# Optimization experiments

Measured on AMD Instinct MI355X. Metric: run time of the kernel, lower is better.

## Reference

```python
import jax, jax.numpy as jnp
import numpy as np

DEPTH = 16
PERCENT = 1.2
MAX_P = 5.0
# ps[t] = clip((t+1)*percent, 0, max_percent), as in the torch __init__
PS = np.clip((np.arange(DEPTH) + 1) * PERCENT, 0.0, MAX_P)


def setup_inputs() -> dict:
    key = jax.random.key(0)
    kx, kA = jax.random.split(key, 2)
    B, M, N = 16384, 256, 1024
    A = jax.random.normal(kA, (M, N), dtype=jnp.float32) / np.sqrt(M)
    # L = max eigenvalue of A^T A (as max_eig in the torch code), scaled by 1.001
    gram = np.asarray(A.T @ A)
    L = float(np.linalg.eigvalsh(gram)[-1]) * 1.001
    # init=True initialization: every bias layer weight is A.T / L, threshold = 1/L
    W = jnp.tile((A.T / L)[None, :, :], (DEPTH, 1, 1))  # [depth, N, M]
    threshold = jnp.ones((DEPTH,), dtype=jnp.float32) / L
    x = jax.random.normal(kx, (B, M), dtype=jnp.float32)
    return {"x": x, "A": A, "W": W, "threshold": threshold}


def _shrink(x, t):
    # soft threshold: sign(x) * max(|x| - t, 0)
    return jnp.sign(x) * jnp.maximum(jnp.abs(x) - t, 0.0)


def _shrinkss(x, t, p):
    # support-selection shrink: entries above both the learned threshold and the
    # per-row (100-p) percentile of |x| pass through untouched; the rest are
    # soft-thresholded. Mask and percentile are detached (no_grad in torch).
    n = x.shape[1]
    idx = int(np.ceil((100.0 - p) / 100.0 * n)) - 1  # static per iteration
    abs_x = jnp.abs(x)
    thresh = jax.lax.stop_gradient(jnp.sort(abs_x, axis=1)[:, idx])  # [B]
    mask = jax.lax.stop_gradient(
        ((abs_x >= t) & (abs_x >= thresh[:, None])).astype(x.dtype)
    )
    return mask * x + _shrink((1.0 - mask) * x, t)


def reference(x, A, W, threshold):
    # x: [B, M], A: [M, N], W: [depth, N, M], threshold: [depth]
    B = x.shape[0]
    N = A.shape[1]
    u = jnp.zeros((B, N), dtype=x.dtype)
    for i in range(DEPTH):
        r = x - u @ A.T                      # residual in measurement space [B, M]
        v = u + r @ W[i].T                   # gradient step via learned bias [B, N]
        u = _shrinkss(v, threshold[i], PS[i])
    return u
```

## Files before the change

### kernel.cpp

```cpp
#include <hip/hip_runtime.h>
#include <hip/hip_bf16.h>

#define B_ROWS 16384
#define M_DIM  256
#define N_DIM  1024
#define DEPTH  16

typedef __attribute__((ext_vector_type(8))) short short8;
typedef __attribute__((ext_vector_type(4))) float f32x4;
typedef __attribute__((ext_vector_type(2))) float f32x2;

#define ATP_OFF_B   0
#define WTP_OFF_B   1572864
#define RP_OFF_B    (1572864 + 25165824)
#define WS_FAST_NEED ((size_t)RP_OFF_B + 25165824)
#define WTP_SLICE   (64 * 8 * 3 * 512)
#define RP_PANEL_US 24576

#define AT_OFF 0
#define WT_OFF (262144)
#define WS_OLD_NEED ((size_t)(262144 + 16 * 262144) * 4)

__device__ __forceinline__ unsigned short bf16r(float f) {
    unsigned u = __float_as_uint(f);
    u += 0x7fffu + ((u >> 16) & 1u);
    return (unsigned short)(u >> 16);
}
__device__ __forceinline__ float bf2f(unsigned short h) {
    return __uint_as_float(((unsigned)h) << 16);
}
__device__ __forceinline__ void split3(float x, unsigned short& h, unsigned short& m,
                                       unsigned short& lo) {
    h = bf16r(x); float r1 = x - bf2f(h);
    m = bf16r(r1); float r2 = r1 - bf2f(m);
    lo = bf16r(r2);
}
__device__ __forceinline__ f32x4 MF(short8 a, short8 b, f32x4 c) {
    return __builtin_amdgcn_mfma_f32_16x16x32_bf16(a, b, c, 0, 0, 0);
}
__device__ __forceinline__ float shrink_one(float v, float t, float thrv) {
    float a = fabsf(v);
    return (a >= thrv) ? v : copysignf(fmaxf(a - t, 0.0f), v);
}

__global__ void prep_a_kernel(const float* __restrict__ A, unsigned short* __restrict__ ATp) {
    int g = blockIdx.x * 256 + threadIdx.x;
    if (g >= 16 * 32 * 64) return;
    int l = g & 63, kc = (g >> 6) & 31, tile = g >> 11;
    int row = tile * 16 + (l & 15);
    int k0 = kc * 32 + ((l >> 4) << 3);
    unsigned short h[8], m[8], lo[8];
#pragma unroll
    for (int j = 0; j < 8; ++j) split3(A[(size_t)row * N_DIM + k0 + j], h[j], m[j], lo[j]);
    size_t base = ((size_t)(tile * 32 + kc) * 3) * 512 + l * 8;
#pragma unroll
    for (int j = 0; j < 8; ++j) {
        ATp[base + j] = h[j];
        ATp[base + 512 + j] = m[j];
        ATp[base + 1024 + j] = lo[j];
    }
}

__global__ void prep_w_kernel(const float* __restrict__ W, unsigned short* __restrict__ WTp) {
    int g = blockIdx.x * 256 + threadIdx.x;
    if (g >= 16 * 64 * 8 * 64) return;
    int l = g & 63, kc = (g >> 6) & 7, tile = (g >> 9) & 63, it = g >> 15;
    int n = tile * 16 + (l & 15);
    int m0 = kc * 32 + ((l >> 4) << 3);
    const float* Wi = W + (size_t)it * N_DIM * M_DIM;
    unsigned short h[8], m[8], lo[8];
#pragma unroll
    for (int j = 0; j < 8; ++j) split3(Wi[(size_t)n * M_DIM + m0 + j], h[j], m[j], lo[j]);
    size_t base = (((size_t)(it * 64 + tile) * 8 + kc) * 3) * 512 + l * 8;
#pragma unroll
    for (int j = 0; j < 8; ++j) {
        WTp[base + j] = h[j];
        WTp[base + 512 + j] = m[j];
        WTp[base + 1024 + j] = lo[j];
    }
}

__global__ void prep_x_kernel(const float* __restrict__ x, unsigned short* __restrict__ RP) {
    int g = blockIdx.x * 256 + threadIdx.x;
    if (g >= 524288) return;
    int l = g & 63, kcp = (g >> 6) & 3, wm = (g >> 8) & 1, c = (g >> 9) & 1, panel = g >> 10;
    int row = panel * 32 + wm * 16 + (l & 15);
    int k0 = c * 128 + kcp * 32 + ((l >> 4) << 3);
    unsigned short h[8], m[8], lo[8];
#pragma unroll
    for (int j = 0; j < 8; ++j) split3(x[(size_t)row * M_DIM + k0 + j], h[j], m[j], lo[j]);
    size_t base = (size_t)panel * RP_PANEL_US + ((((c * 2 + wm) * 4 + kcp) * 3)) * 512 + l * 8;
#pragma unroll
    for (int j = 0; j < 8; ++j) {
        RP[base + j] = h[j];
        RP[base + 512 + j] = m[j];
        RP[base + 1024 + j] = lo[j];
    }
}

__global__ __launch_bounds__(1024)
void spp_kernel(float* __restrict__ UV, const float* __restrict__ thr_all,
                int iter, int kth) {
    const int l = threadIdx.x & 63;
    const int w = threadIdx.x >> 6;
    const int row = blockIdx.x * 16 + w;
    const float t = thr_all[iter];
    float* vp = UV + (size_t)row * N_DIM;
    float v[16]; unsigned key[16];
#pragma unroll
    for (int j = 0; j < 16; ++j) {
        v[j] = vp[l + 64 * j];
        key[j] = __float_as_uint(v[j]) & 0x7fffffffu;
    }
    unsigned p = 0;
#pragma unroll 1
    for (int b = 30; b >= 0; --b) {
        const unsigned cand = p | (1u << b);
        int cnt = 0;
#pragma unroll
        for (int j = 0; j < 16; ++j)
            cnt += __popcll(__ballot(key[j] >= cand));
        if (cnt >= kth) p = cand;
    }
    const float thrv = fmaxf(t, __uint_as_float(p));
#pragma unroll
    for (int j = 0; j < 16; ++j)
        vp[l + 64 * j] = shrink_one(v[j], t, thrv);
}

#define LSTR2 136
#define BUFUS 13056

__global__ __launch_bounds__(1024)
void g1_kernel(const float* __restrict__ UV, const float* __restrict__ x,
               const unsigned short* __restrict__ ATp,
               unsigned short* __restrict__ RP) {
    __align__(16) __shared__ unsigned short smem[2 * BUFUS];
    const int tid = threadIdx.x;
    const int l = tid & 63, w = tid >> 6;
    const int wm = w >> 3, wn = w & 7;
    const int panel = blockIdx.x;
    const int row0 = panel * 32;
    const int arow = 16 * wm + (l & 15);
    const int akl  = (l >> 4) << 3;

    f32x4 acc_hi[2], acc_rest[2];
    double acc64[2][4];
#pragma unroll
    for (int t = 0; t < 2; ++t) {
        acc_hi[t] = (f32x4){0, 0, 0, 0};
        acc_rest[t] = (f32x4){0, 0, 0, 0};
#pragma unroll
        for (int e = 0; e < 4; ++e) acc64[t][e] = 0.0;
    }

    f32x2 st[2];
#pragma unroll
    for (int jj = 0; jj < 2; ++jj) {
        const int idx = tid + 1024 * jj;
        const int r = idx >> 6, kq = idx & 63;
        st[jj] = *(const f32x2*)&UV[(size_t)(row0 + r) * N_DIM + kq * 2];
    }
#pragma unroll
    for (int jj = 0; jj < 2; ++jj) {
        const int idx = tid + 1024 * jj;
        const int r = idx >> 6, kq = idx & 63;
        unsigned short h0, m0, lo0, h1, m1, lo1;
        split3(st[jj].x, h0, m0, lo0);
        split3(st[jj].y, h1, m1, lo1);
        const unsigned off = (unsigned)r * LSTR2 + kq * 2;
        *(unsigned*)&smem[off] = (unsigned)h0 | ((unsigned)h1 << 16);
        *(unsigned*)&smem[4352 + off] = (unsigned)m0 | ((unsigned)m1 << 16);
        *(unsigned*)&smem[8704 + off] = (unsigned)lo0 | ((unsigned)lo1 << 16);
    }
#pragma unroll
    for (int jj = 0; jj < 2; ++jj) {
        const int idx = tid + 1024 * jj;
        const int r = idx >> 6, kq = idx & 63;
        st[jj] = *(const f32x2*)&UV[(size_t)(row0 + r) * N_DIM + 128 + kq * 2];
    }
    __syncthreads();

    for (int c = 0; c < 8; ++c) {
        const unsigned bb = (unsigned)(c & 1) * BUFUS;
        const unsigned nb = (unsigned)((c + 1) & 1) * BUFUS;
        if (c < 7) {
#pragma unroll
            for (int jj = 0; jj < 2; ++jj) {
                const int idx = tid + 1024 * jj;
                const int r = idx >> 6, kq = idx & 63;
                unsigned short h0, m0, lo0, h1, m1, lo1;
                split3(st[jj].x, h0, m0, lo0);
                split3(st[jj].y, h1, m1, lo1);
                const unsigned off = (unsigned)r * LSTR2 + kq * 2;
                *(unsigned*)&smem[nb + off] = (unsigned)h0 | ((unsigned)h1 << 16);
                *(unsigned*)&smem[nb + 4352 + off] = (unsigned)m0 | ((unsigned)m1 << 16);
                *(unsigned*)&smem[nb + 8704 + off] = (unsigned)lo0 | ((unsigned)lo1 << 16);
            }
        }
        if (c < 6) {
#pragma unroll
            for (int jj = 0; jj < 2; ++jj) {
                const int idx = tid + 1024 * jj;
                const int r = idx >> 6, kq = idx & 63;
                st[jj] = *(const f32x2*)&UV[(size_t)(row0 + r) * N_DIM + (c + 2) * 128 + kq * 2];
            }
        }
#pragma unroll
        for (int kc = 0; kc < 4; ++kc) {
            const unsigned ao = bb + (unsigned)arow * LSTR2 + kc * 32 + akl;
            short8 ah = *(const short8*)&smem[ao];
            short8 am = *(const short8*)&smem[ao + 4352];
            short8 al = *(const short8*)&smem[ao + 8704];
#pragma unroll
            for (int tt = 0; tt < 2; ++tt) {
                const int tile = wn * 2 + tt;
                const unsigned bo = ((unsigned)(tile * 32 + c * 4 + kc) * 3) * 512 + l * 8;
                short8 bh = *(const short8*)&ATp[bo];
                short8 bm = *(const short8*)&ATp[bo + 512];
                short8 bl = *(const short8*)&ATp[bo + 1024];
                acc_hi[tt] = MF(ah, bh, acc_hi[tt]);
                acc_rest[tt] = MF(ah, bm, acc_rest[tt]);
                acc_rest[tt] = MF(am, bh, acc_rest[tt]);
                acc_rest[tt] = MF(am, bm, acc_rest[tt]);
                acc_rest[tt] = MF(ah, bl, acc_rest[tt]);
                acc_rest[tt] = MF(al, bh, acc_rest[tt]);
            }
        }
#pragma unroll
        for (int tt = 0; tt < 2; ++tt) {
#pragma unroll
            for (int e = 0; e < 4; ++e) acc64[tt][e] += (double)acc_hi[tt][e];
            acc_hi[tt] = (f32x4){0, 0, 0, 0};
        }
        __syncthreads();
    }

    {
        const int cimg = wn >> 2, kcp = wn & 3;
        const unsigned fbase = ((((unsigned)(cimg * 2 + wm) * 4 + kcp) * 3)) * 512;
#pragma unroll
        for (int tt = 0; tt < 2; ++tt) {
            const int col = wn * 32 + tt * 16 + (l & 15);
            const int hi2 = (tt * 2 + ((l & 15) >> 3)) & 3;
#pragma unroll
            for (int e = 0; e < 4; ++e) {
                const int rl = ((l >> 4) << 2) + e;
                const int row = row0 + wm * 16 + rl;
                const double tot = acc64[tt][e] + (double)acc_rest[tt][e];
                const float rv = (float)((double)x[(size_t)row * M_DIM + col] - tot);
                unsigned short h, m, lo;
                split3(rv, h, m, lo);
                const unsigned sl = fbase + (unsigned)(hi2 * 16 + rl) * 8 + (l & 7);
                smem[sl] = h;
                smem[sl + 512] = m;
                smem[sl + 1024] = lo;
            }
        }
    }
    __syncthreads();
    {
        const uint4* s4 = (const uint4*)smem;
        uint4* d4 = (uint4*)(RP + (size_t)panel * RP_PANEL_US);
        d4[tid] = s4[tid];
        d4[tid + 1024] = s4[tid + 1024];
        d4[tid + 2048] = s4[tid + 2048];
    }
}

__global__ __launch_bounds__(1024)
void g2_kernel(const unsigned short* __restrict__ RP, const unsigned short* __restrict__ WTpi,
               float* UV, int iter) {
    __align__(16) __shared__ unsigned short img[24576];
    const int tid = threadIdx.x;
    const int l = tid & 63, w = tid >> 6;
    const int wm = w >> 3, wn = w & 7;
    const int panel = blockIdx.x >> 2, cg = blockIdx.x & 3;
    const int row0 = panel * 32;

    {
        const uint4* s4 = (const uint4*)(RP + (size_t)panel * RP_PANEL_US);
        uint4* d4 = (uint4*)img;
        d4[tid] = s4[tid];
        d4[tid + 1024] = s4[tid + 1024];
        d4[tid + 2048] = s4[tid + 2048];
    }
    __syncthreads();

    f32x4 hi[2], rest[2], sum[2];
#pragma unroll
    for (int t = 0; t < 2; ++t) {
        hi[t] = (f32x4){0, 0, 0, 0};
        rest[t] = (f32x4){0, 0, 0, 0};
        sum[t] = (f32x4){0, 0, 0, 0};
    }

    for (int kc = 0; kc < 8; ++kc) {
        const unsigned ab = ((((unsigned)(kc >> 2) * 2 + wm) * 4 + (kc & 3)) * 3) * 512 + l * 8;
        short8 ah = *(const short8*)&img[ab];
        short8 am = *(const short8*)&img[ab + 512];
        short8 al = *(const short8*)&img[ab + 1024];
#pragma unroll
        for (int tt = 0; tt < 2; ++tt) {
            const int tile = cg * 16 + wn * 2 + tt;
            const unsigned bo = ((unsigned)(tile * 8 + kc) * 3) * 512 + l * 8;
            short8 bh = *(const short8*)&WTpi[bo];
            short8 bm = *(const short8*)&WTpi[bo + 512];
            short8 bl = *(const short8*)&WTpi[bo + 1024];
            hi[tt] = MF(ah, bh, hi[tt]);
            rest[tt] = MF(ah, bm, rest[tt]);
            rest[tt] = MF(am, bh, rest[tt]);
            rest[tt] = MF(am, bm, rest[tt]);
            rest[tt] = MF(ah, bl, rest[tt]);
            rest[tt] = MF(al, bh, rest[tt]);
        }
        if ((kc & 3) == 3) {
#pragma unroll
            for (int tt = 0; tt < 2; ++tt) {
#pragma unroll
                for (int e = 0; e < 4; ++e) sum[tt][e] += hi[tt][e];
                hi[tt] = (f32x4){0, 0, 0, 0};
            }
        }
    }

#pragma unroll
    for (int tt = 0; tt < 2; ++tt) {
        const int col = cg * 256 + wn * 32 + tt * 16 + (l & 15);
#pragma unroll
        for (int e = 0; e < 4; ++e) {
            const int row = row0 + wm * 16 + ((l >> 4) << 2) + e;
            const float tot = sum[tt][e] + rest[tt][e];
            const float us = (iter > 0) ? UV[(size_t)row * N_DIM + col] : 0.0f;
            UV[(size_t)row * N_DIM + col] = us + tot;
        }
    }
}

__global__ __launch_bounds__(256)
void s_kernel(float* UV, const float* __restrict__ thr_all, int iter, int kth) {
    __shared__ float v_s[8][1024];
    __shared__ float tau_s[8];
    const int tid = threadIdx.x;
    const int lane = tid & 63;
    const int wave = tid >> 6;
    const int row0 = blockIdx.x * 8;
    const float t = thr_all[iter];
    {
        const float4* Vg4 = (const float4*)(UV + (size_t)row0 * N_DIM);
        float4* vs4 = (float4*)(&v_s[0][0]);
#pragma unroll
        for (int c = 0; c < 8; ++c) vs4[tid + 256 * c] = Vg4[tid + 256 * c];
    }
    __syncthreads();
#pragma unroll 1
    for (int rr = 0; rr < 2; ++rr) {
        const int row = wave + rr * 4;
        unsigned key[16];
#pragma unroll
        for (int j = 0; j < 16; ++j)
            key[j] = __float_as_uint(v_s[row][lane + 64 * j]) & 0x7fffffffu;
        unsigned p = 0;
#pragma unroll 1
        for (int b = 30; b >= 0; --b) {
            const unsigned cand = p | (1u << b);
            int cnt = 0;
#pragma unroll
            for (int j = 0; j < 16; ++j) cnt += (key[j] >= cand) ? 1 : 0;
#pragma unroll
            for (int off = 32; off; off >>= 1) cnt += __shfl_xor(cnt, off);
            if (cnt >= kth) p = cand;
        }
        if (lane == 0) tau_s[row] = __uint_as_float(p);
    }
    __syncthreads();
    {
        const float4* vs4 = (const float4*)&v_s[0][0];
        float4* Uw = (float4*)(UV + (size_t)row0 * N_DIM);
#pragma unroll 1
        for (int c = 0; c < 8; ++c) {
            const int idx = tid + 256 * c;
            const int row = idx >> 8;
            const float thrv = fmaxf(t, tau_s[row]);
            float4 v = vs4[idx];
            float4 o;
            o.x = shrink_one(v.x, t, thrv);
            o.y = shrink_one(v.y, t, thrv);
            o.z = shrink_one(v.z, t, thrv);
            o.w = shrink_one(v.w, t, thrv);
            Uw[idx] = o;
        }
    }
}

#define DFMA4(acc, s, v) do { \
    (acc).x += (double)(s) * (double)(v).x; \
    (acc).y += (double)(s) * (double)(v).y; \
    (acc).z += (double)(s) * (double)(v).z; \
    (acc).w += (double)(s) * (double)(v).w; } while (0)

__global__ void transpose_kernel(const float* __restrict__ in, float* __restrict__ out,
                                 int R, int C) {
    __shared__ float tile[32][33];
    int s = blockIdx.z;
    const float* ip = in + (size_t)s * R * C;
    float* op = out + (size_t)s * R * C;
    int c0 = blockIdx.x * 32, r0 = blockIdx.y * 32;
    int tx = threadIdx.x, ty = threadIdx.y;
#pragma unroll
    for (int k = 0; k < 4; ++k)
        tile[ty + 8 * k][tx] = ip[(size_t)(r0 + ty + 8 * k) * C + (c0 + tx)];
    __syncthreads();
#pragma unroll
    for (int k = 0; k < 4; ++k)
        op[(size_t)(c0 + ty + 8 * k) * R + (r0 + tx)] = tile[tx][ty + 8 * k];
}

__global__ void zero_kernel(float* __restrict__ p, int n) {
    int i = blockIdx.x * blockDim.x + threadIdx.x;
    int stride = gridDim.x * blockDim.x;
    for (; i < n; i += stride) p[i] = 0.0f;
}

template <bool T>
__device__ __forceinline__ float4 loadAT(const float* __restrict__ p, int n, int m4) {
    if constexpr (T) {
        return ((const float4*)p)[n * 64 + m4];
    } else {
        float4 r;
        r.x = p[(size_t)(4 * m4 + 0) * N_DIM + n];
        r.y = p[(size_t)(4 * m4 + 1) * N_DIM + n];
        r.z = p[(size_t)(4 * m4 + 2) * N_DIM + n];
        r.w = p[(size_t)(4 * m4 + 3) * N_DIM + n];
        return r;
    }
}
template <bool T>
__device__ __forceinline__ float4 loadWT(const float* __restrict__ p, int m, int n4) {
    if constexpr (T) {
        return ((const float4*)p)[m * 256 + n4];
    } else {
        float4 r;
        r.x = p[(size_t)(4 * n4 + 0) * M_DIM + m];
        r.y = p[(size_t)(4 * n4 + 1) * M_DIM + m];
        r.z = p[(size_t)(4 * n4 + 2) * M_DIM + m];
        r.w = p[(size_t)(4 * n4 + 3) * M_DIM + m];
        return r;
    }
}

template <bool T>
__global__ __launch_bounds__(256)
void lista_iter_kernel(const float* __restrict__ x, const float* __restrict__ Ap,
                       const float* __restrict__ Wp, const float* __restrict__ thr_all,
                       float* __restrict__ U, int iter, int kth) {
    __shared__ float u_s[8][1024];
    __shared__ float r_s[8][256];
    __shared__ float tau_s[8];
    const int tid = threadIdx.x;
    const int lane = tid & 63;
    const int wave = tid >> 6;
    const int row0 = blockIdx.x * 8;
    const float t = thr_all[iter];
    {
        const float4* Ug4 = (const float4*)(U + (size_t)row0 * N_DIM);
        float4* us4 = (float4*)(&u_s[0][0]);
#pragma unroll
        for (int c = 0; c < 8; ++c) us4[tid + 256 * c] = Ug4[tid + 256 * c];
    }
    __syncthreads();
    {
        double4 acc0 = {0, 0, 0, 0}, acc1 = {0, 0, 0, 0};
        const float4* u0p = (const float4*)&u_s[wave][0];
        const float4* u1p = (const float4*)&u_s[wave + 4][0];
        for (int n4 = 0; n4 < 256; ++n4) {
            float4 u0 = u0p[n4];
            float4 u1 = u1p[n4];
            float4 a0 = loadAT<T>(Ap, 4 * n4 + 0, lane);
            float4 a1 = loadAT<T>(Ap, 4 * n4 + 1, lane);
            float4 a2 = loadAT<T>(Ap, 4 * n4 + 2, lane);
            float4 a3 = loadAT<T>(Ap, 4 * n4 + 3, lane);
            DFMA4(acc0, u0.x, a0); DFMA4(acc0, u0.y, a1); DFMA4(acc0, u0.z, a2); DFMA4(acc0, u0.w, a3);
            DFMA4(acc1, u1.x, a0); DFMA4(acc1, u1.y, a1); DFMA4(acc1, u1.z, a2); DFMA4(acc1, u1.w, a3);
        }
        float4 xv0 = ((const float4*)(x + (size_t)(row0 + wave) * M_DIM))[lane];
        float4 xv1 = ((const float4*)(x + (size_t)(row0 + wave + 4) * M_DIM))[lane];
        float4 rv0, rv1;
        rv0.x = (float)((double)xv0.x - acc0.x);
        rv0.y = (float)((double)xv0.y - acc0.y);
        rv0.z = (float)((double)xv0.z - acc0.z);
        rv0.w = (float)((double)xv0.w - acc0.w);
        rv1.x = (float)((double)xv1.x - acc1.x);
        rv1.y = (float)((double)xv1.y - acc1.y);
        rv1.z = (float)((double)xv1.z - acc1.z);
        rv1.w = (float)((double)xv1.w - acc1.w);
        ((float4*)&r_s[wave][0])[lane] = rv0;
        ((float4*)&r_s[wave + 4][0])[lane] = rv1;
    }
    __syncthreads();
    {
        const float4* r0p = (const float4*)&r_s[wave][0];
        const float4* r1p = (const float4*)&r_s[wave + 4][0];
        float4* u0p = (float4*)&u_s[wave][0];
        float4* u1p = (float4*)&u_s[wave + 4][0];
#pragma unroll 1
        for (int q = 0; q < 4; ++q) {
            const int n4 = lane + 64 * q;
            double4 acc0 = {0, 0, 0, 0}, acc1 = {0, 0, 0, 0};
            for (int m4 = 0; m4 < 64; ++m4) {
                float4 r0 = r0p[m4];
                float4 r1 = r1p[m4];
                float4 w0 = loadWT<T>(Wp, 4 * m4 + 0, n4);
                float4 w1 = loadWT<T>(Wp, 4 * m4 + 1, n4);
                float4 w2 = loadWT<T>(Wp, 4 * m4 + 2, n4);
                float4 w3 = loadWT<T>(Wp, 4 * m4 + 3, n4);
                DFMA4(acc0, r0.x, w0); DFMA4(acc0, r0.y, w1); DFMA4(acc0, r0.z, w2); DFMA4(acc0, r0.w, w3);
                DFMA4(acc1, r1.x, w0); DFMA4(acc1, r1.y, w1); DFMA4(acc1, r1.z, w2); DFMA4(acc1, r1.w, w3);
            }
            float4 uv0 = u0p[n4];
            uv0.x = (float)((double)uv0.x + acc0.x);
            uv0.y = (float)((double)uv0.y + acc0.y);
            uv0.z = (float)((double)uv0.z + acc0.z);
            uv0.w = (float)((double)uv0.w + acc0.w);
            u0p[n4] = uv0;
            float4 uv1 = u1p[n4];
            uv1.x = (float)((double)uv1.x + acc1.x);
            uv1.y = (float)((double)uv1.y + acc1.y);
            uv1.z = (float)((double)uv1.z + acc1.z);
            uv1.w = (float)((double)uv1.w + acc1.w);
            u1p[n4] = uv1;
        }
    }
    __syncthreads();
    {
#pragma unroll 1
        for (int rr = 0; rr < 2; ++rr) {
            const int row = wave + rr * 4;
            unsigned key[16];
#pragma unroll
            for (int j = 0; j < 16; ++j)
                key[j] = __float_as_uint(u_s[row][lane + 64 * j]) & 0x7fffffffu;
            unsigned p = 0;
#pragma unroll 1
            for (int b = 30; b >= 0; --b) {
                const unsigned cand = p | (1u << b);
                int cnt = 0;
#pragma unroll
                for (int j = 0; j < 16; ++j) cnt += (key[j] >= cand) ? 1 : 0;
#pragma unroll
                for (int off = 32; off; off >>= 1) cnt += __shfl_xor(cnt, off);
                if (cnt >= kth) p = cand;
            }
            if (lane == 0) tau_s[row] = __uint_as_float(p);
        }
    }
    __syncthreads();
    {
        const float4* us4 = (const float4*)&u_s[0][0];
        float4* Uw = (float4*)(U + (size_t)row0 * N_DIM);
#pragma unroll 1
        for (int c = 0; c < 8; ++c) {
            const int idx = tid + 256 * c;
            const int row = idx >> 8;
            const float thrv = fmaxf(t, tau_s[row]);
            float4 v = us4[idx];
            float4 o;
            o.x = shrink_one(v.x, t, thrv);
            o.y = shrink_one(v.y, t, thrv);
            o.z = shrink_one(v.z, t, thrv);
            o.w = shrink_one(v.w, t, thrv);
            Uw[idx] = o;
        }
    }
}

extern "C" void kernel_launch(void* const* d_in, const int* in_sizes, int n_in,
                              void* d_out, int out_size, void* d_ws, size_t ws_size,
                              hipStream_t stream) {
    const float* x   = (const float*)d_in[0];
    const float* A   = (const float*)d_in[1];
    const float* W   = (const float*)d_in[2];
    const float* thr = (const float*)d_in[3];

    float* UV = (float*)d_out;

    static const int ktab[DEPTH] = {13, 25, 37, 50, 52, 52, 52, 52,
                                    52, 52, 52, 52, 52, 52, 52, 52};

    if (ws_size >= WS_FAST_NEED) {
        unsigned short* ATp = (unsigned short*)((char*)d_ws + ATP_OFF_B);
        unsigned short* WTp = (unsigned short*)((char*)d_ws + WTP_OFF_B);
        unsigned short* RP  = (unsigned short*)((char*)d_ws + RP_OFF_B);

        prep_a_kernel<<<128, 256, 0, stream>>>(A, ATp);
        prep_w_kernel<<<2048, 256, 0, stream>>>(W, WTp);
        prep_x_kernel<<<2048, 256, 0, stream>>>(x, RP);

        g2_kernel<<<2048, 1024, 0, stream>>>(RP, WTp, UV, 0);

        for (int it = 1; it < DEPTH; ++it) {
            spp_kernel<<<B_ROWS / 16, 1024, 0, stream>>>(UV, thr, it - 1, ktab[it - 1]);
            g1_kernel<<<512, 1024, 0, stream>>>(UV, x, ATp, RP);
            g2_kernel<<<2048, 1024, 0, stream>>>(RP, WTp + (size_t)it * WTP_SLICE, UV, it);
        }
        s_kernel<<<B_ROWS / 8, 256, 0, stream>>>(UV, thr, DEPTH - 1, ktab[DEPTH - 1]);
    } else if (ws_size >= WS_OLD_NEED) {
        float* ws = (float*)d_ws;
        float* AT = ws + AT_OFF;
        float* WT = ws + WT_OFF;
        zero_kernel<<<1024, 256, 0, stream>>>(UV, B_ROWS * N_DIM);
        dim3 tb(32, 8);
        transpose_kernel<<<dim3(N_DIM / 32, M_DIM / 32, 1), tb, 0, stream>>>(A, AT, M_DIM, N_DIM);
        transpose_kernel<<<dim3(M_DIM / 32, N_DIM / 32, DEPTH), tb, 0, stream>>>(W, WT, N_DIM, M_DIM);
        for (int it = 0; it < DEPTH; ++it)
            lista_iter_kernel<true><<<B_ROWS / 8, 256, 0, stream>>>(
                x, AT, WT + (size_t)it * M_DIM * N_DIM, thr, UV, it, ktab[it]);
    } else {
        zero_kernel<<<1024, 256, 0, stream>>>(UV, B_ROWS * N_DIM);
        for (int it = 0; it < DEPTH; ++it)
            lista_iter_kernel<false><<<B_ROWS / 8, 256, 0, stream>>>(
                x, A, W + (size_t)it * N_DIM * M_DIM, thr, UV, it, ktab[it]);
    }
}
```

Before: 3.127 ms.

## Split g1 residual GEMM into 16-row panels with 512-thread blocks

The g1 kernel now processes 16 rows per block with 8 waves instead of 32 rows with 16 waves, launching 1024 blocks instead of 512. Each wave covers two column tiles of A^T for all 16 rows, and the output scatter is rewritten to place each half-panel into the existing 32-row RP layout. The goal is more blocks for better CU occupancy and load balance with half the LDS per block. In exchange, each ATp tile is reloaded by twice as many blocks, adding global and L2 traffic.

```diff
diff --git a/kernel.cpp b/kernel.cpp
--- a/kernel.cpp
+++ b/kernel.cpp
@@ -129,19 +129,18 @@
 }
 
 #define LSTR2 136
-#define BUFUS 13056
-
-__global__ __launch_bounds__(1024)
+#define BUF16 6528
+
+__global__ __launch_bounds__(512)
 void g1_kernel(const float* __restrict__ UV, const float* __restrict__ x,
                const unsigned short* __restrict__ ATp,
                unsigned short* __restrict__ RP) {
-    __align__(16) __shared__ unsigned short smem[2 * BUFUS];
+    __align__(16) __shared__ unsigned short smem[2 * BUF16];
     const int tid = threadIdx.x;
     const int l = tid & 63, w = tid >> 6;
-    const int wm = w >> 3, wn = w & 7;
-    const int panel = blockIdx.x;
-    const int row0 = panel * 32;
-    const int arow = 16 * wm + (l & 15);
+    const int panel16 = blockIdx.x;
+    const int row0 = panel16 * 16;
+    const int arow = l & 15;
     const int akl  = (l >> 4) << 3;
 
     f32x4 acc_hi[2], acc_rest[2];
@@ -157,51 +156,51 @@
     f32x2 st[2];
 #pragma unroll
     for (int jj = 0; jj < 2; ++jj) {
-        const int idx = tid + 1024 * jj;
+        const int idx = tid + 512 * jj;
         const int r = idx >> 6, kq = idx & 63;
         st[jj] = *(const f32x2*)&UV[(size_t)(row0 + r) * N_DIM + kq * 2];
     }
 #pragma unroll
     for (int jj = 0; jj < 2; ++jj) {
-        const int idx = tid + 1024 * jj;
+        const int idx = tid + 512 * jj;
         const int r = idx >> 6, kq = idx & 63;
         unsigned short h0, m0, lo0, h1, m1, lo1;
         split3(st[jj].x, h0, m0, lo0);
         split3(st[jj].y, h1, m1, lo1);
         const unsigned off = (unsigned)r * LSTR2 + kq * 2;
         *(unsigned*)&smem[off] = (unsigned)h0 | ((unsigned)h1 << 16);
-        *(unsigned*)&smem[4352 + off] = (unsigned)m0 | ((unsigned)m1 << 16);
-        *(unsigned*)&smem[8704 + off] = (unsigned)lo0 | ((unsigned)lo1 << 16);
+        *(unsigned*)&smem[2176 + off] = (unsigned)m0 | ((unsigned)m1 << 16);
+        *(unsigned*)&smem[4352 + off] = (unsigned)lo0 | ((unsigned)lo1 << 16);
     }
 #pragma unroll
     for (int jj = 0; jj < 2; ++jj) {
-        const int idx = tid + 1024 * jj;
+        const int idx = tid + 512 * jj;
         const int r = idx >> 6, kq = idx & 63;
         st[jj] = *(const f32x2*)&UV[(size_t)(row0 + r) * N_DIM + 128 + kq * 2];
     }
     __syncthreads();
 
     for (int c = 0; c < 8; ++c) {
-        const unsigned bb = (unsigned)(c & 1) * BUFUS;
-        const unsigned nb = (unsigned)((c + 1) & 1) * BUFUS;
+        const unsigned bb = (unsigned)(c & 1) * BUF16;
+        const unsigned nb = (unsigned)((c + 1) & 1) * BUF16;
         if (c < 7) {
 #pragma unroll
             for (int jj = 0; jj < 2; ++jj) {
-                const int idx = tid + 1024 * jj;
+                const int idx = tid + 512 * jj;
                 const int r = idx >> 6, kq = idx & 63;
                 unsigned short h0, m0, lo0, h1, m1, lo1;
                 split3(st[jj].x, h0, m0, lo0);
                 split3(st[jj].y, h1, m1, lo1);
                 const unsigned off = (unsigned)r * LSTR2 + kq * 2;
                 *(unsigned*)&smem[nb + off] = (unsigned)h0 | ((unsigned)h1 << 16);
-                *(unsigned*)&smem[nb + 4352 + off] = (unsigned)m0 | ((unsigned)m1 << 16);
-                *(unsigned*)&smem[nb + 8704 + off] = (unsigned)lo0 | ((unsigned)lo1 << 16);
+                *(unsigned*)&smem[nb + 2176 + off] = (unsigned)m0 | ((unsigned)m1 << 16);
+                *(unsigned*)&smem[nb + 4352 + off] = (unsigned)lo0 | ((unsigned)lo1 << 16);
             }
         }
         if (c < 6) {
 #pragma unroll
             for (int jj = 0; jj < 2; ++jj) {
-                const int idx = tid + 1024 * jj;
+                const int idx = tid + 512 * jj;
                 const int r = idx >> 6, kq = idx & 63;
                 st[jj] = *(const f32x2*)&UV[(size_t)(row0 + r) * N_DIM + (c + 2) * 128 + kq * 2];
             }
@@ -210,11 +209,11 @@
         for (int kc = 0; kc < 4; ++kc) {
             const unsigned ao = bb + (unsigned)arow * LSTR2 + kc * 32 + akl;
             short8 ah = *(const short8*)&smem[ao];
-            short8 am = *(const short8*)&smem[ao + 4352];
-            short8 al = *(const short8*)&smem[ao + 8704];
+            short8 am = *(const short8*)&smem[ao + 2176];
+            short8 al = *(const short8*)&smem[ao + 4352];
 #pragma unroll
             for (int tt = 0; tt < 2; ++tt) {
-                const int tile = wn * 2 + tt;
+                const int tile = w * 2 + tt;
                 const unsigned bo = ((unsigned)(tile * 32 + c * 4 + kc) * 3) * 512 + l * 8;
                 short8 bh = *(const short8*)&ATp[bo];
                 short8 bm = *(const short8*)&ATp[bo + 512];
@@ -237,21 +236,22 @@
     }
 
     {
-        const int cimg = wn >> 2, kcp = wn & 3;
-        const unsigned fbase = ((((unsigned)(cimg * 2 + wm) * 4 + kcp) * 3)) * 512;
 #pragma unroll
         for (int tt = 0; tt < 2; ++tt) {
-            const int col = wn * 32 + tt * 16 + (l & 15);
-            const int hi2 = (tt * 2 + ((l & 15) >> 3)) & 3;
+            const int ki = (w * 2 + tt) * 16 + (l & 15);
+            const unsigned c_  = (unsigned)ki >> 7;
+            const unsigned kcp = ((unsigned)ki >> 5) & 3;
+            const unsigned hi2 = ((unsigned)ki >> 3) & 3;
+            const unsigned fbase = ((c_ * 4 + kcp) * 3) * 512;
 #pragma unroll
             for (int e = 0; e < 4; ++e) {
-                const int rl = ((l >> 4) << 2) + e;
-                const int row = row0 + wm * 16 + rl;
+                const int mi = ((l >> 4) << 2) + e;
+                const int row = row0 + mi;
                 const double tot = acc64[tt][e] + (double)acc_rest[tt][e];
-                const float rv = (float)((double)x[(size_t)row * M_DIM + col] - tot);
+                const float rv = (float)((double)x[(size_t)row * M_DIM + ki] - tot);
                 unsigned short h, m, lo;
                 split3(rv, h, m, lo);
-                const unsigned sl = fbase + (unsigned)(hi2 * 16 + rl) * 8 + (l & 7);
+                const unsigned sl = fbase + (unsigned)(hi2 * 16 + mi) * 8 + (ki & 7);
                 smem[sl] = h;
                 smem[sl + 512] = m;
                 smem[sl + 1024] = lo;
@@ -260,11 +260,18 @@
     }
     __syncthreads();
     {
+        const int wm = panel16 & 1;
+        const int panel32 = panel16 >> 1;
         const uint4* s4 = (const uint4*)smem;
-        uint4* d4 = (uint4*)(RP + (size_t)panel * RP_PANEL_US);
-        d4[tid] = s4[tid];
-        d4[tid + 1024] = s4[tid + 1024];
-        d4[tid + 2048] = s4[tid + 2048];
+#pragma unroll
+        for (int qq = 0; qq < 3; ++qq) {
+            const int q = tid + 512 * qq;
+            const int c_ = (q >= 768) ? 1 : 0;
+            const int off = q - c_ * 768;
+            uint4* d4 = (uint4*)(RP + (size_t)panel32 * RP_PANEL_US +
+                                 (size_t)(c_ * 2 + wm) * 6144);
+            d4[off] = s4[q];
+        }
     }
 }
 
@@ -600,7 +607,7 @@
 
         for (int it = 1; it < DEPTH; ++it) {
             spp_kernel<<<B_ROWS / 16, 1024, 0, stream>>>(UV, thr, it - 1, ktab[it - 1]);
-            g1_kernel<<<512, 1024, 0, stream>>>(UV, x, ATp, RP);
+            g1_kernel<<<B_ROWS / 16, 512, 0, stream>>>(UV, x, ATp, RP);
             g2_kernel<<<2048, 1024, 0, stream>>>(RP, WTp + (size_t)it * WTP_SLICE, UV, it);
         }
         s_kernel<<<B_ROWS / 8, 256, 0, stream>>>(UV, thr, DEPTH - 1, ktab[DEPTH - 1]);
```

Measured after the change: 3.181 ms. About the same (+1.7%).
